# Kernel optimization log

Measured on AMD Instinct MI355X. Metric: run time of the kernel, lower is better.

The kernel has to match this reference:

```python
import jax, jax.numpy as jnp
import numpy as np

ROPE_THETA = 10000.0

def apply_rope(x, positions):
    # x: [b, h, s, d], positions: [s]
    d = x.shape[-1]
    inv_freq = ROPE_THETA ** (-jnp.arange(0, d, 2, dtype=jnp.float32) / d)  # [d/2]
    ang = positions.astype(jnp.float32)[:, None] * inv_freq[None, :]        # [s, d/2]
    cos = jnp.cos(ang)
    sin = jnp.sin(ang)
    x1 = x[..., 0::2]
    x2 = x[..., 1::2]
    r1 = x1 * cos - x2 * sin
    r2 = x1 * sin + x2 * cos
    # interleave back to [..., d]
    return jnp.stack([r1, r2], axis=-1).reshape(x.shape)

def setup_inputs() -> dict:
    key = jax.random.key(0)
    k1, k2, k3 = jax.random.split(key, 3)
    b, s, d_model = 4, 2048, 1024
    x = jax.random.normal(k1, (b, s, d_model), dtype=jnp.float32)
    wqkv = jax.random.normal(k2, (3 * d_model, d_model), dtype=jnp.float32) * (d_model ** -0.5)
    wo = jax.random.normal(k3, (d_model, d_model), dtype=jnp.float32) * (d_model ** -0.5)
    token_positions = jnp.arange(s, dtype=jnp.int64 if jax.config.jax_enable_x64 else jnp.int32)
    return {"x": x, "wqkv": wqkv, "wo": wo, "token_positions": token_positions}

def reference(x, wqkv, wo, token_positions):
    b, s, d_model = x.shape
    num_heads = 16
    d_head = d_model // num_heads
    # fused QKV projection (Linear: y = x @ W.T)
    qkv = jnp.einsum('bse,fe->bsf', x, wqkv)  # [b, s, 3*d_model]
    q, k, v = jnp.split(qkv, 3, axis=-1)
    def to_heads(t):
        return t.reshape(b, s, num_heads, d_head).transpose(0, 2, 1, 3)  # [b, h, s, d]
    q, k, v = to_heads(q), to_heads(k), to_heads(v)
    q = apply_rope(q, token_positions)
    k = apply_rope(k, token_positions)
    scores = jnp.einsum('bhqd,bhkd->bhqk', q, k) / jnp.sqrt(jnp.asarray(d_head, dtype=x.dtype))
    causal = jnp.tril(jnp.ones((s, s), dtype=bool))  # [s, s]
    scores = jnp.where(causal, scores, -jnp.inf)
    weights = jax.nn.softmax(scores, axis=-1)
    y = jnp.einsum('bhqk,bhkd->bhqd', weights, v)
    y = y.transpose(0, 2, 1, 3).reshape(b, s, d_model)
    return jnp.einsum('bse,fe->bsf', y, wo)
```

## Files before the change

### kernel.cpp

```cpp
#include <hip/hip_runtime.h>
#include <stdint.h>


typedef __attribute__((ext_vector_type(8))) short bf16x8;
typedef __attribute__((ext_vector_type(4))) float f32x4;
typedef __attribute__((ext_vector_type(8))) unsigned short u16x8;
typedef __attribute__((ext_vector_type(4))) unsigned short u16x4;
typedef __attribute__((ext_vector_type(4))) unsigned int u32x4;

#define NB 4
#define NS 2048
#define NH 16
#define DH 64
#define DM 1024
#define BH (NB*NH)

static __device__ __forceinline__ unsigned short f2bf(float f){
  unsigned u = __builtin_bit_cast(unsigned, f);
  u += 0x7fffu + ((u >> 16) & 1u);
  return (unsigned short)(u >> 16);
}
static __device__ __forceinline__ float bf2f(unsigned short h){
  unsigned u = ((unsigned)h) << 16;
  return __builtin_bit_cast(float, u);
}
static __device__ __forceinline__ unsigned cvt_pk_bf16(float lo, float hi){
  unsigned r;
  asm("v_cvt_pk_bf16_f32 %0, %1, %2" : "=v"(r) : "v"(lo), "v"(hi));
  return r;
}
static __device__ __forceinline__ f32x4 mfma16(bf16x8 a, bf16x8 b, f32x4 c){
  return __builtin_amdgcn_mfma_f32_16x16x32_bf16(a, b, c, 0, 0, 0);
}
static __device__ __forceinline__ void gld_lds16(const void* g, void* l){
  __builtin_amdgcn_global_load_lds((const __attribute__((address_space(1))) unsigned int*)g,
                                   (__attribute__((address_space(3))) unsigned int*)l,
                                   16, 0, 0);
}

__global__ __launch_bounds__(256) void cvt_all(const float* __restrict__ x,
                                               const float* __restrict__ wqkv,
                                               const float* __restrict__ wo,
                                               const int* __restrict__ pos,
                                               unsigned short* __restrict__ xb,
                                               unsigned short* __restrict__ wqkvb,
                                               unsigned short* __restrict__ wob,
                                               float* __restrict__ ct,
                                               float* __restrict__ st){
  int stride = gridDim.x * blockDim.x;
  for (int i = blockIdx.x * blockDim.x + threadIdx.x; i < 3211264; i += stride){
    if (i < 3145728){
      const float* src; unsigned short* dst; int j;
      if (i < 2097152){ src = x; dst = xb; j = i; }
      else if (i < 2883584){ src = wqkv; dst = wqkvb; j = i - 2097152; }
      else { src = wo; dst = wob; j = i - 2883584; }
      f32x4 v = *(const f32x4*)(src + (size_t)j * 4);
      u16x4 o;
      o[0] = f2bf(v[0]); o[1] = f2bf(v[1]); o[2] = f2bf(v[2]); o[3] = f2bf(v[3]);
      *(u16x4*)(dst + (size_t)j * 4) = o;
    } else {
      int t = i - 3145728;
      int s = t >> 5, fi = t & 31;
      float p = (float)pos[s];
      float freq = exp2f(-(float)(2 * fi) * (13.287712379549449f / 64.f));
      float a = p * freq;
      ct[t] = cosf(a);
      st[t] = sinf(a);
    }
  }
}

template<int BM, int BN, int MF, int NFR, int EPI, int RING, int OCC>
__global__ __launch_bounds__((BM/(MF*16))*(BN/(NFR*16))*64, OCC)
void gemm_ring(const unsigned short* __restrict__ A,
               const unsigned short* __restrict__ Bm,
               void* __restrict__ out0, void* __restrict__ out1,
               void* __restrict__ out2,
               const float* __restrict__ ct_, const float* __restrict__ st_,
               int M, int N, int K){
  constexpr int WM = BM / (MF * 16);
  constexpr int WN = BN / (NFR * 16);
  constexpr int T  = WM * WN * 64;
  constexpr int LA = BM * 4 / T;
  constexpr int LB = BN * 4 / T;
  constexpr int L  = LA + LB;
  constexpr unsigned RB = (unsigned)RING * (BM + BN) * 64;
  constexpr unsigned EB = (EPI == 0) ? (unsigned)(128 * 132 * 2) : 0u;
  constexpr unsigned SB = RB > EB ? RB : EB;
  __shared__ __attribute__((aligned(16))) unsigned char smem[SB];
  unsigned short* As = (unsigned short*)smem;
  unsigned short* Bs = As + (size_t)RING * BM * 32;
  int tid = threadIdx.x;
  int w = tid >> 6, l = tid & 63;
  int lr = l & 15, lk = l >> 4;
  int m0 = blockIdx.y * BM, n0 = blockIdx.x * BN;
  int wr = (w / WN) * (MF * 16), wc = (w % WN) * (NFR * 16);

  const int nt = K >> 5;

  auto stage = [&](int t, int buf){
    int k0 = t * 32;
#pragma unroll
    for (int i = 0; i < LA; i++){
      int f = i * T + tid;
      int row = f >> 2, c = f & 3;
      int gc = (c ^ ((row >> 1) & 3)) * 8;
      gld_lds16(A + (size_t)(m0 + row) * K + k0 + gc, &As[(size_t)buf * BM * 32 + (i * T + w * 64) * 8]);
    }
#pragma unroll
    for (int i = 0; i < LB; i++){
      int f = i * T + tid;
      int row = f >> 2, c = f & 3;
      int gc = (c ^ ((row >> 1) & 3)) * 8;
      gld_lds16(Bm + (size_t)(n0 + row) * K + k0 + gc, &Bs[(size_t)buf * BN * 32 + (i * T + w * 64) * 8]);
    }
  };

  f32x4 zero = {0.f, 0.f, 0.f, 0.f};
  f32x4 acc[MF][NFR];
#pragma unroll
  for (int a = 0; a < MF; a++)
#pragma unroll
    for (int b = 0; b < NFR; b++) acc[a][b] = zero;

#pragma unroll
  for (int p = 0; p < RING - 1; p++) stage(p, p);
  asm volatile("s_waitcnt vmcnt(%0)" :: "i"((RING - 2) * L) : "memory");
  __builtin_amdgcn_sched_barrier(0);
  __builtin_amdgcn_s_barrier();
  __builtin_amdgcn_sched_barrier(0);

  int buf = 0;
  for (int t = 0; t < nt; ++t){
    bf16x8 af[MF], bfr[NFR];
#pragma unroll
    for (int mf = 0; mf < MF; mf++){
      int row = wr + mf * 16 + lr;
      af[mf] = *(const bf16x8*)&As[(size_t)buf * BM * 32 + row * 32 + ((lk ^ ((row >> 1) & 3)) * 8)];
    }
#pragma unroll
    for (int nf = 0; nf < NFR; nf++){
      int row = wc + nf * 16 + lr;
      bfr[nf] = *(const bf16x8*)&Bs[(size_t)buf * BN * 32 + row * 32 + ((lk ^ ((row >> 1) & 3)) * 8)];
    }
    if (t + RING - 1 < nt){
      int sb = buf - 1; if (sb < 0) sb = RING - 1;
      stage(t + RING - 1, sb);
    }
    __builtin_amdgcn_s_setprio(1);
#pragma unroll
    for (int mf = 0; mf < MF; mf++)
#pragma unroll
      for (int nf = 0; nf < NFR; nf++)
        acc[mf][nf] = mfma16(af[mf], bfr[nf], acc[mf][nf]);
    __builtin_amdgcn_s_setprio(0);
    if (RING >= 4){
      if (t + 3 < nt)      { asm volatile("s_waitcnt vmcnt(%0)" :: "i"(2 * L) : "memory"); }
      else if (t + 2 < nt) { asm volatile("s_waitcnt vmcnt(%0)" :: "i"(L) : "memory"); }
      else if (t + 1 < nt) { asm volatile("s_waitcnt vmcnt(0)" ::: "memory"); }
    } else {
      if (t + 2 < nt)      { asm volatile("s_waitcnt vmcnt(%0)" :: "i"(L) : "memory"); }
      else if (t + 1 < nt) { asm volatile("s_waitcnt vmcnt(0)" ::: "memory"); }
    }
    __builtin_amdgcn_sched_barrier(0);
    __builtin_amdgcn_s_barrier();
    __builtin_amdgcn_sched_barrier(0);
    buf = buf + 1; if (buf == RING) buf = 0;
  }

  if (EPI == 0){
    unsigned short* q  = (unsigned short*)out0;
    unsigned short* k  = (unsigned short*)out1;
    unsigned short* vt = (unsigned short*)out2;
    unsigned short* sm = (unsigned short*)smem;
    int part = n0 >> 10;
    int b = m0 >> 11;
    __syncthreads();
    if (part == 2){
#pragma unroll
      for (int mf = 0; mf < MF; mf++)
#pragma unroll
        for (int nf = 0; nf < NFR; nf++)
#pragma unroll
          for (int j = 0; j < 4; j++)
            sm[(wc + nf * 16 + lr) * 130 + (wr + mf * 16 + lk * 4 + j)] = f2bf(acc[mf][nf][j]);
      __syncthreads();
      int nrow = tid >> 1, mh = tid & 1;
      int n = n0 + nrow;
      int h = (n & 1023) >> 6, dh = n & 63;
      int s0 = (m0 & (NS - 1)) + mh * 64;
      unsigned short* dst = vt + ((size_t)((b * NH + h) * DH + dh)) * NS + s0;
      const unsigned short* srcr = &sm[nrow * 130 + mh * 64];
#pragma unroll
      for (int ch = 0; ch < 4; ch++)
        *(u16x8*)(dst + ch * 8 + ((mh ^ 0) & 0) ) = *(const u16x8*)(srcr + ch * 8);
#pragma unroll
      for (int ch = 4; ch < 8; ch++)
        *(u16x8*)(dst + ch * 8) = *(const u16x8*)(srcr + ch * 8);
    } else {
#pragma unroll
      for (int mf = 0; mf < MF; mf++)
#pragma unroll
        for (int nf = 0; nf < NFR; nf++)
#pragma unroll
          for (int j = 0; j < 4; j++)
            sm[(wr + mf * 16 + lk * 4 + j) * 132 + (wc + nf * 16 + lr)] = f2bf(acc[mf][nf][j]);
      __syncthreads();
      int mrow = tid >> 1, hh = tid & 1;
      int s = (m0 + mrow) & (NS - 1);
      int c0 = (n0 & 1023) + hh * 64;
      int h = c0 >> 6;
      unsigned short* dst = ((part == 0) ? q : k) + ((size_t)((b * NH + h) * NS + s)) * DH;
      const unsigned short* srcr = &sm[mrow * 132 + hh * 64];
      if (part == 1){
        const float* ctr = ct_ + s * 32;
        const float* str = st_ + s * 32;
#pragma unroll
        for (int ch = 0; ch < 8; ch++){
          u16x8 v = *(const u16x8*)(srcr + ch * 8);
          f32x4 cc = *(const f32x4*)(ctr + ch * 4);
          f32x4 ss = *(const f32x4*)(str + ch * 4);
          u16x8 o;
#pragma unroll
          for (int p = 0; p < 4; p++){
            float x1 = bf2f(v[2*p]), x2 = bf2f(v[2*p+1]);
            o[2*p]   = f2bf(x1 * cc[p] - x2 * ss[p]);
            o[2*p+1] = f2bf(x1 * ss[p] + x2 * cc[p]);
          }
          *(u16x8*)(dst + ch * 8) = o;
        }
      } else {
#pragma unroll
        for (int ch = 0; ch < 8; ch++)
          *(u16x8*)(dst + ch * 8) = *(const u16x8*)(srcr + ch * 8);
      }
    }
  } else {
    float* C = (float*)out0;
#pragma unroll
    for (int mf = 0; mf < MF; mf++)
#pragma unroll
      for (int nf = 0; nf < NFR; nf++)
#pragma unroll
        for (int j = 0; j < 4; j++){
          int m = m0 + wr + mf * 16 + lk * 4 + j;
          int n = n0 + wc + nf * 16 + lr;
          C[(size_t)m * N + n] = acc[mf][nf][j];
        }
  }
}

__global__ __launch_bounds__(256, 3) void fa_kernel(const unsigned short* __restrict__ qb_,
                                                    const unsigned short* __restrict__ kbuf,
                                                    const unsigned short* __restrict__ vtb,
                                                    unsigned short* __restrict__ yb,
                                                    const float* __restrict__ ct_,
                                                    const float* __restrict__ st_){
  __shared__ __attribute__((aligned(16))) unsigned short Kl[2][4096];
  __shared__ __attribute__((aligned(16))) unsigned short Vl[2][4096];
  __shared__ __attribute__((aligned(16))) unsigned short Pl[4][32 * 76];
  int tid = threadIdx.x;
  int w = tid >> 6, l = tid & 63;
  int lr = l & 15, lk = l >> 4;
  int qb = 15 - blockIdx.y;
  int bh = blockIdx.x;
  int b = bh >> 4, h = bh & 15;
  int qr0 = qb * 128 + w * 32;
  const unsigned short* Q  = qb_  + (size_t)bh * NS * DH;
  const unsigned short* Kp = kbuf + (size_t)bh * NS * DH;
  const unsigned short* VT = vtb  + (size_t)bh * DH * NS;
  unsigned short* Pw = &Pl[w][0];

  int r8  = l >> 3;
  int swc = ((l & 7) ^ (r8 & 7)) * 8;

  auto stage = [&](int buf, int t){
    int kbase = t * 64;
    if (w < 2){
#pragma unroll
      for (int ii = 0; ii < 4; ii++){
        int i = w * 4 + ii;
        gld_lds16(Kp + (size_t)(kbase + i * 8 + r8) * DH + swc, &Kl[buf][i * 512]);
      }
    } else {
#pragma unroll
      for (int ii = 0; ii < 4; ii++){
        int i = (w - 2) * 4 + ii;
        gld_lds16(VT + (size_t)(i * 8 + r8) * NS + kbase + swc, &Vl[buf][i * 512]);
      }
    }
  };

  const float SC = 0.18033688011112042f;
  bf16x8 qf[2][2];
#pragma unroll
  for (int mf = 0; mf < 2; mf++){
    int srow = qr0 + mf * 16 + lr;
    const unsigned short* qrow = Q + (size_t)srow * DH;
    const float* ctr = ct_ + srow * 32;
    const float* str = st_ + srow * 32;
#pragma unroll
    for (int ks = 0; ks < 2; ks++){
      u16x8 raw = *(const u16x8*)(qrow + ks * 32 + lk * 8);
      f32x4 cc = *(const f32x4*)(ctr + ks * 16 + lk * 4);
      f32x4 ss = *(const f32x4*)(str + ks * 16 + lk * 4);
      u32x4 wds;
#pragma unroll
      for (int p = 0; p < 4; p++){
        float c2 = cc[p] * SC, s2 = ss[p] * SC;
        float x1 = bf2f(raw[2*p]), x2 = bf2f(raw[2*p+1]);
        wds[p] = cvt_pk_bf16(x1 * c2 - x2 * s2, x1 * s2 + x2 * c2);
      }
      qf[mf][ks] = __builtin_bit_cast(bf16x8, wds);
    }
  }

  bf16x8 ones;
#pragma unroll
  for (int p = 0; p < 8; p++) ones[p] = (short)0x3F80;

  f32x4 zero = {0.f, 0.f, 0.f, 0.f};
  f32x4 O[2][4];
  f32x4 Ls[2];
#pragma unroll
  for (int mf = 0; mf < 2; mf++){
#pragma unroll
    for (int nf = 0; nf < 4; nf++) O[mf][nf] = zero;
    Ls[mf] = zero;
  }

  const int ntile = 2 * qb + 2;

  stage(0, 0);
  __syncthreads();

  int cur = 0;
  for (int t = 0; t < ntile; ++t){
    int kbase = t * 64;
    if (t + 1 < ntile) stage(cur ^ 1, t + 1);

    if (kbase <= qr0 + 31){
      bf16x8 kf[4][2];
#pragma unroll
      for (int nf = 0; nf < 4; nf++){
        int row = nf * 16 + lr;
        int ro = row * 64, sw = (row & 7) << 3;
#pragma unroll
        for (int ks = 0; ks < 2; ks++)
          kf[nf][ks] = *(const bf16x8*)&Kl[cur][ro + ((ks * 32 + lk * 8) ^ sw)];
      }
      bf16x8 vf[2][4];
#pragma unroll
      for (int nfd = 0; nfd < 4; nfd++){
        int row = nfd * 16 + lr;
        int ro = row * 64, sw = (row & 7) << 3;
#pragma unroll
        for (int ks = 0; ks < 2; ks++)
          vf[ks][nfd] = *(const bf16x8*)&Vl[cur][ro + ((ks * 32 + lk * 8) ^ sw)];
      }

      f32x4 sa[2][4];
#pragma unroll
      for (int mf = 0; mf < 2; mf++)
#pragma unroll
        for (int nf = 0; nf < 4; nf++) sa[mf][nf] = zero;
#pragma unroll
      for (int nf = 0; nf < 4; nf++)
#pragma unroll
        for (int mf = 0; mf < 2; mf++){
          sa[mf][nf] = mfma16(kf[nf][0], qf[mf][0], sa[mf][nf]);
          sa[mf][nf] = mfma16(kf[nf][1], qf[mf][1], sa[mf][nf]);
        }

      bool domask = (kbase + 63 > qr0);

#pragma unroll
      for (int mf = 0; mf < 2; mf++){
        int qg = qr0 + mf * 16 + lr;
#pragma unroll
        for (int nf = 0; nf < 4; nf++){
          float p4[4];
#pragma unroll
          for (int j = 0; j < 4; j++){
            float xx = sa[mf][nf][j];
            if (domask){
              int kg = kbase + nf * 16 + lk * 4 + j;
              if (kg > qg) xx = -__builtin_inff();
            }
            p4[j] = exp2f(xx);
          }
          unsigned d0 = cvt_pk_bf16(p4[0], p4[1]);
          unsigned d1 = cvt_pk_bf16(p4[2], p4[3]);
          int base = (mf * 16 + lr) * 76 + nf * 16 + lk * 4;
          *(unsigned*)&Pw[base]     = d0;
          *(unsigned*)&Pw[base + 2] = d1;
        }
      }

      bf16x8 pf[2][2];
#pragma unroll
      for (int mf = 0; mf < 2; mf++)
#pragma unroll
        for (int ks = 0; ks < 2; ks++)
          pf[mf][ks] = *(const bf16x8*)&Pw[(mf * 16 + lr) * 76 + ks * 32 + lk * 8];
#pragma unroll
      for (int ks = 0; ks < 2; ks++)
#pragma unroll
        for (int nfd = 0; nfd < 4; nfd++)
#pragma unroll
          for (int mf = 0; mf < 2; mf++)
            O[mf][nfd] = mfma16(pf[mf][ks], vf[ks][nfd], O[mf][nfd]);
#pragma unroll
      for (int ks = 0; ks < 2; ks++)
#pragma unroll
        for (int mf = 0; mf < 2; mf++)
          Ls[mf] = mfma16(pf[mf][ks], ones, Ls[mf]);
    }

    __syncthreads();
    cur ^= 1;
  }

#pragma unroll
  for (int mf = 0; mf < 2; mf++)
#pragma unroll
    for (int j = 0; j < 4; j++){
      float inv = 1.0f / Ls[mf][j];
      int srow = qr0 + mf * 16 + lk * 4 + j;
      unsigned short* yp = yb + ((size_t)(b * NS + srow)) * DM + h * DH;
#pragma unroll
      for (int nfd = 0; nfd < 4; nfd++)
        yp[nfd * 16 + lr] = f2bf(O[mf][nfd][j] * inv);
    }
}

extern "C" void kernel_launch(void* const* d_in, const int* in_sizes, int n_in,
                              void* d_out, int out_size, void* d_ws, size_t ws_size,
                              hipStream_t stream){
  const float* x    = (const float*)d_in[0];
  const float* wqkv = (const float*)d_in[1];
  const float* wo   = (const float*)d_in[2];
  const int*   pos  = (const int*)d_in[3];
  float* out = (float*)d_out;

  char* ws = (char*)d_ws;
  size_t off = 0;
  auto alloc = [&](size_t bytes) -> void* {
    void* p = ws + off;
    off += (bytes + 255) & ~(size_t)255;
    return p;
  };
  const size_t NE = (size_t)BH * NS * DH;
  unsigned short* xb    = (unsigned short*)alloc((size_t)8192 * 1024 * 2);
  unsigned short* wqkvb = (unsigned short*)alloc((size_t)3072 * 1024 * 2);
  unsigned short* wob   = (unsigned short*)alloc((size_t)1024 * 1024 * 2);
  unsigned short* q  = (unsigned short*)alloc(NE * 2);
  unsigned short* k  = (unsigned short*)alloc(NE * 2);
  unsigned short* vt = (unsigned short*)alloc(NE * 2);
  unsigned short* y  = (unsigned short*)alloc(NE * 2);
  float* ct = (float*)alloc((size_t)NS * 32 * 4);
  float* st = (float*)alloc((size_t)NS * 32 * 4);

  cvt_all<<<3072, 256, 0, stream>>>(x, wqkv, wo, pos, xb, wqkvb, wob, ct, st);
  gemm_ring<128, 128, 4, 4, 0, 3, 3><<<dim3(24, 64), 256, 0, stream>>>(
      xb, wqkvb, q, k, vt, ct, st, 8192, 3072, 1024);
  fa_kernel<<<dim3(64, 16), 256, 0, stream>>>(q, k, vt, y, ct, st);
  gemm_ring<128, 128, 4, 4, 1, 4, 2><<<dim3(8, 64), 256, 0, stream>>>(
      y, wob, out, nullptr, nullptr, nullptr, nullptr, 8192, 1024, 1024);
}
```

Measured before the change: 188.2 us.

## Double attention query tile per block to reuse staged K/V tiles

The flash-attention kernel now processes 256 query rows per block (64 per wave) instead of 128, halving the grid and doubling reuse of each staged K/V tile. Score computation is restructured per 16-row fragment, and V fragments are loaded from LDS inside the PV loop to limit register pressure. Launch bounds drop to 2 blocks/CU and the P scratch buffer doubles. The block schedule also changes so the heaviest causal tiles go first. Fewer blocks and more registers may reduce occupancy and load balance.

New measurement: 221.0 us. +17.4%, slower.

```diff
diff --git a/kernel.cpp b/kernel.cpp
--- a/kernel.cpp
+++ b/kernel.cpp
@@ -192,10 +192,7 @@
       unsigned short* dst = vt + ((size_t)((b * NH + h) * DH + dh)) * NS + s0;
       const unsigned short* srcr = &sm[nrow * 130 + mh * 64];
 #pragma unroll
-      for (int ch = 0; ch < 4; ch++)
-        *(u16x8*)(dst + ch * 8 + ((mh ^ 0) & 0) ) = *(const u16x8*)(srcr + ch * 8);
-#pragma unroll
-      for (int ch = 4; ch < 8; ch++)
+      for (int ch = 0; ch < 8; ch++)
         *(u16x8*)(dst + ch * 8) = *(const u16x8*)(srcr + ch * 8);
     } else {
 #pragma unroll
@@ -250,7 +247,7 @@
   }
 }
 
-__global__ __launch_bounds__(256, 3) void fa_kernel(const unsigned short* __restrict__ qb_,
+__global__ __launch_bounds__(256, 2) void fa_kernel(const unsigned short* __restrict__ qb_,
                                                     const unsigned short* __restrict__ kbuf,
                                                     const unsigned short* __restrict__ vtb,
                                                     unsigned short* __restrict__ yb,
@@ -258,14 +255,15 @@
                                                     const float* __restrict__ st_){
   __shared__ __attribute__((aligned(16))) unsigned short Kl[2][4096];
   __shared__ __attribute__((aligned(16))) unsigned short Vl[2][4096];
-  __shared__ __attribute__((aligned(16))) unsigned short Pl[4][32 * 76];
+  __shared__ __attribute__((aligned(16))) unsigned short Pl[4][64 * 76];
   int tid = threadIdx.x;
   int w = tid >> 6, l = tid & 63;
   int lr = l & 15, lk = l >> 4;
-  int qb = 15 - blockIdx.y;
+  int yb_ = blockIdx.y;
+  int qb = (yb_ < 4) ? (7 - yb_) : (yb_ - 4);
   int bh = blockIdx.x;
   int b = bh >> 4, h = bh & 15;
-  int qr0 = qb * 128 + w * 32;
+  int qr0 = qb * 256 + w * 64;
   const unsigned short* Q  = qb_  + (size_t)bh * NS * DH;
   const unsigned short* Kp = kbuf + (size_t)bh * NS * DH;
   const unsigned short* VT = vtb  + (size_t)bh * DH * NS;
@@ -292,9 +290,9 @@
   };
 
   const float SC = 0.18033688011112042f;
-  bf16x8 qf[2][2];
-#pragma unroll
-  for (int mf = 0; mf < 2; mf++){
+  bf16x8 qf[4][2];
+#pragma unroll
+  for (int mf = 0; mf < 4; mf++){
     int srow = qr0 + mf * 16 + lr;
     const unsigned short* qrow = Q + (size_t)srow * DH;
     const float* ctr = ct_ + srow * 32;
@@ -320,16 +318,16 @@
   for (int p = 0; p < 8; p++) ones[p] = (short)0x3F80;
 
   f32x4 zero = {0.f, 0.f, 0.f, 0.f};
-  f32x4 O[2][4];
-  f32x4 Ls[2];
-#pragma unroll
-  for (int mf = 0; mf < 2; mf++){
+  f32x4 O[4][4];
+  f32x4 Ls[4];
+#pragma unroll
+  for (int mf = 0; mf < 4; mf++){
 #pragma unroll
     for (int nf = 0; nf < 4; nf++) O[mf][nf] = zero;
     Ls[mf] = zero;
   }
 
-  const int ntile = 2 * qb + 2;
+  const int ntile = 4 * qb + 4;
 
   stage(0, 0);
   __syncthreads();
@@ -339,7 +337,7 @@
     int kbase = t * 64;
     if (t + 1 < ntile) stage(cur ^ 1, t + 1);
 
-    if (kbase <= qr0 + 31){
+    if (kbase <= qr0 + 63){
       bf16x8 kf[4][2];
 #pragma unroll
       for (int nf = 0; nf < 4; nf++){
@@ -349,40 +347,25 @@
         for (int ks = 0; ks < 2; ks++)
           kf[nf][ks] = *(const bf16x8*)&Kl[cur][ro + ((ks * 32 + lk * 8) ^ sw)];
       }
-      bf16x8 vf[2][4];
-#pragma unroll
-      for (int nfd = 0; nfd < 4; nfd++){
-        int row = nfd * 16 + lr;
-        int ro = row * 64, sw = (row & 7) << 3;
-#pragma unroll
-        for (int ks = 0; ks < 2; ks++)
-          vf[ks][nfd] = *(const bf16x8*)&Vl[cur][ro + ((ks * 32 + lk * 8) ^ sw)];
-      }
-
-      f32x4 sa[2][4];
-#pragma unroll
-      for (int mf = 0; mf < 2; mf++)
-#pragma unroll
-        for (int nf = 0; nf < 4; nf++) sa[mf][nf] = zero;
-#pragma unroll
-      for (int nf = 0; nf < 4; nf++)
-#pragma unroll
-        for (int mf = 0; mf < 2; mf++){
-          sa[mf][nf] = mfma16(kf[nf][0], qf[mf][0], sa[mf][nf]);
-          sa[mf][nf] = mfma16(kf[nf][1], qf[mf][1], sa[mf][nf]);
+      bool domask = (kbase + 63 > qr0);
+
+#pragma unroll
+      for (int mf = 0; mf < 4; mf++){
+        f32x4 sa[4];
+#pragma unroll
+        for (int nf = 0; nf < 4; nf++) sa[nf] = zero;
+#pragma unroll
+        for (int nf = 0; nf < 4; nf++){
+          sa[nf] = mfma16(kf[nf][0], qf[mf][0], sa[nf]);
+          sa[nf] = mfma16(kf[nf][1], qf[mf][1], sa[nf]);
         }
-
-      bool domask = (kbase + 63 > qr0);
-
-#pragma unroll
-      for (int mf = 0; mf < 2; mf++){
         int qg = qr0 + mf * 16 + lr;
 #pragma unroll
         for (int nf = 0; nf < 4; nf++){
           float p4[4];
 #pragma unroll
           for (int j = 0; j < 4; j++){
-            float xx = sa[mf][nf][j];
+            float xx = sa[nf][j];
             if (domask){
               int kg = kbase + nf * 16 + lk * 4 + j;
               if (kg > qg) xx = -__builtin_inff();
@@ -397,23 +380,27 @@
         }
       }
 
-      bf16x8 pf[2][2];
-#pragma unroll
-      for (int mf = 0; mf < 2; mf++)
+      bf16x8 pf[4][2];
+#pragma unroll
+      for (int mf = 0; mf < 4; mf++)
 #pragma unroll
         for (int ks = 0; ks < 2; ks++)
           pf[mf][ks] = *(const bf16x8*)&Pw[(mf * 16 + lr) * 76 + ks * 32 + lk * 8];
 #pragma unroll
       for (int ks = 0; ks < 2; ks++)
 #pragma unroll
-        for (int nfd = 0; nfd < 4; nfd++)
-#pragma unroll
-          for (int mf = 0; mf < 2; mf++)
-            O[mf][nfd] = mfma16(pf[mf][ks], vf[ks][nfd], O[mf][nfd]);
+        for (int nfd = 0; nfd < 4; nfd++){
+          int row = nfd * 16 + lr;
+          int ro = row * 64, sw = (row & 7) << 3;
+          bf16x8 vf = *(const bf16x8*)&Vl[cur][ro + ((ks * 32 + lk * 8) ^ sw)];
+#pragma unroll
+          for (int mf = 0; mf < 4; mf++)
+            O[mf][nfd] = mfma16(pf[mf][ks], vf, O[mf][nfd]);
+        }
 #pragma unroll
       for (int ks = 0; ks < 2; ks++)
 #pragma unroll
-        for (int mf = 0; mf < 2; mf++)
+        for (int mf = 0; mf < 4; mf++)
           Ls[mf] = mfma16(pf[mf][ks], ones, Ls[mf]);
     }
 
@@ -422,7 +409,7 @@
   }
 
 #pragma unroll
-  for (int mf = 0; mf < 2; mf++)
+  for (int mf = 0; mf < 4; mf++)
 #pragma unroll
     for (int j = 0; j < 4; j++){
       float inv = 1.0f / Ls[mf][j];
@@ -464,7 +451,7 @@
   cvt_all<<<3072, 256, 0, stream>>>(x, wqkv, wo, pos, xb, wqkvb, wob, ct, st);
   gemm_ring<128, 128, 4, 4, 0, 3, 3><<<dim3(24, 64), 256, 0, stream>>>(
       xb, wqkvb, q, k, vt, ct, st, 8192, 3072, 1024);
-  fa_kernel<<<dim3(64, 16), 256, 0, stream>>>(q, k, vt, y, ct, st);
+  fa_kernel<<<dim3(64, 8), 256, 0, stream>>>(q, k, vt, y, ct, st);
   gemm_ring<128, 128, 4, 4, 1, 4, 2><<<dim3(8, 64), 256, 0, stream>>>(
       y, wob, out, nullptr, nullptr, nullptr, nullptr, 8192, 1024, 1024);
 }
```
